# Kernel tuning notes

Hardware: AMD Instinct MI355X
Metric: run time of the kernel (lower is better)

The kernel has to match this reference:

```python
import jax, jax.numpy as jnp
import numpy as np

N_NODES = 100000
N_EDGES = 3200000
IN_DIM, HID_DIM, OUT_DIM = 128, 64, 2


def setup_inputs() -> dict:
    key = jax.random.key(0)
    k1, k2, k3, k4 = jax.random.split(key, 4)
    x = jax.random.normal(k1, (N_NODES, IN_DIM), dtype=jnp.float32)
    edge_index = jax.random.randint(k2, (2, N_EDGES), 0, N_NODES, dtype=jnp.int64)
    # GCNConv weights (glorot-style scale) and zero biases
    W1 = jax.random.normal(k3, (IN_DIM, HID_DIM), dtype=jnp.float32) / np.sqrt(IN_DIM)
    b1 = jnp.zeros((HID_DIM,), dtype=jnp.float32)
    W2 = jax.random.normal(k4, (HID_DIM, OUT_DIM), dtype=jnp.float32) / np.sqrt(HID_DIM)
    b2 = jnp.zeros((OUT_DIM,), dtype=jnp.float32)
    return {"x": x, "edge_index": edge_index, "W1": W1, "b1": b1, "W2": W2, "b2": b2}


def _gcn_norm(edge_index, num_nodes):
    # PyG GCNConv default: add self-loops, symmetric normalization deg^-1/2.
    loops = jnp.arange(num_nodes, dtype=edge_index.dtype)
    src = jnp.concatenate([edge_index[0], loops])  # [E+N]
    dst = jnp.concatenate([edge_index[1], loops])  # [E+N]
    deg = jax.ops.segment_sum(jnp.ones_like(dst, dtype=jnp.float32), dst,
                              num_segments=num_nodes)  # in-degree incl. self-loop
    dinv = jnp.where(deg > 0, jax.lax.rsqrt(deg), 0.0)
    norm = dinv[src] * dinv[dst]  # [E+N]
    return src, dst, norm


def _gcn_conv(h, W, b, src, dst, norm, num_nodes):
    h = h @ W                              # dense transform first (smaller dim)
    msg = h[src] * norm[:, None]           # gather + scale: [E+N, d]
    out = jax.ops.segment_sum(msg, dst, num_segments=num_nodes)  # scatter-add
    return out + b


def reference(x, edge_index, W1, b1, W2, b2):
    n = x.shape[0]
    src, dst, norm = _gcn_norm(edge_index, n)
    h = _gcn_conv(x, W1, b1, src, dst, norm, n)
    h = jax.nn.relu(h)
    return _gcn_conv(h, W2, b2, src, dst, norm, n)
```

## Files before the change

kernel.cpp:

```cpp
#include <hip/hip_runtime.h>
#include <hip/hip_bf16.h>


#define N_NODES 100000
#define IN_DIM 128
#define HID_DIM 64
#define OUT_DIM 2
#define NB 391
#define BCAP 12288
#define CROUNDS 12
#define CHUNK 8192
#define ZROW N_NODES

typedef short bf16x8 __attribute__((ext_vector_type(8)));
typedef float f32x4 __attribute__((ext_vector_type(4)));

__device__ __forceinline__ unsigned short f2bf(float x) {
    unsigned int u = __float_as_uint(x);
    unsigned int r = (u + 0x7FFFu + ((u >> 16) & 1u)) >> 16;
    return (unsigned short)r;
}
__device__ __forceinline__ float bflo(unsigned int u) { return __uint_as_float(u << 16); }
__device__ __forceinline__ float bfhi(unsigned int u) { return __uint_as_float(u & 0xFFFF0000u); }
__device__ __forceinline__ f32x4 vlo(uint4 r) {
    return (f32x4){bflo(r.x), bflo(r.y), bflo(r.z), bflo(r.w)};
}
__device__ __forceinline__ f32x4 vhi(uint4 r) {
    return (f32x4){bfhi(r.x), bfhi(r.y), bfhi(r.z), bfhi(r.w)};
}
__device__ __forceinline__ int wave_incl_scan(int v, int laneid) {
#pragma unroll
    for (int off = 1; off < 64; off <<= 1) {
        int u = __shfl_up(v, off);
        if (laneid >= off) v += u;
    }
    return v;
}

__global__ __launch_bounds__(512) void part_kernel(const int* __restrict__ ei,
                                                   int* __restrict__ gCursor,
                                                   int* __restrict__ part, int E) {
    __shared__ int hist[512], lrow[512], gbase[512], lcur[512];
    __shared__ int lpk[CHUNK];
    __shared__ short lbkt[CHUNK];
    __shared__ int wsum[8], wofs[8];
    const int t = threadIdx.x;
    const int lane = t & 63, wv = t >> 6;
    const int base = blockIdx.x * CHUNK;
    const int cntC = min(CHUNK, E - base);

    hist[t] = 0;
    __syncthreads();

    int s[16], d[16];
    bool val[16];
    if (base + CHUNK <= E) {
#pragma unroll
        for (int i = 0; i < 4; ++i) {
            int4 sv = ((const int4*)(ei + base))[t + i * 512];
            int4 dv = ((const int4*)(ei + E + base))[t + i * 512];
            s[i * 4 + 0] = sv.x; s[i * 4 + 1] = sv.y; s[i * 4 + 2] = sv.z; s[i * 4 + 3] = sv.w;
            d[i * 4 + 0] = dv.x; d[i * 4 + 1] = dv.y; d[i * 4 + 2] = dv.z; d[i * 4 + 3] = dv.w;
            val[i * 4 + 0] = val[i * 4 + 1] = val[i * 4 + 2] = val[i * 4 + 3] = true;
        }
    } else {
#pragma unroll
        for (int i = 0; i < 16; ++i) {
            int e = base + t + i * 512;
            val[i] = (e < E);
            if (val[i]) {
                s[i] = ei[e];
                d[i] = ei[E + e];
            }
        }
    }
#pragma unroll
    for (int i = 0; i < 16; ++i)
        if (val[i]) atomicAdd(&hist[d[i] >> 8], 1);
    __syncthreads();

    int v = hist[t];
    int inc = wave_incl_scan(v, lane);
    if (lane == 63) wsum[wv] = inc;
    __syncthreads();
    if (t < 64) {
        int w = (t < 8) ? wsum[t] : 0;
        int wi = wave_incl_scan(w, t);
        if (t < 8) wofs[t] = wi - w;
    }
    __syncthreads();
    int excl = inc - v + wofs[wv];
    if (t < NB && v > 0) {
        int old = atomicAdd(&gCursor[t], v);
        gbase[t] = t * BCAP + old;
    }
    lcur[t] = excl;
    lrow[t] = excl;
    __syncthreads();

#pragma unroll
    for (int i = 0; i < 16; ++i) {
        if (val[i]) {
            int b = d[i] >> 8;
            int pos = atomicAdd(&lcur[b], 1);
            lpk[pos] = s[i] | ((d[i] & 255) << 20);
            lbkt[pos] = (short)b;
        }
    }
    __syncthreads();

    for (int i = t; i < cntC; i += 512) {
        int b = lbkt[i];
        int g = gbase[b] + (i - lrow[b]);
        if (g < (b + 1) * BCAP)
            part[g] = lpk[i];
    }
}

__global__ __launch_bounds__(1024) void csr_kernel(const int* __restrict__ part,
                                                   const int* __restrict__ gCursor,
                                                   int* __restrict__ cnt,
                                                   float* __restrict__ dinv,
                                                   int* __restrict__ rowptr,
                                                   int* __restrict__ csr_src, int n) {
    __shared__ int wcnt[16][256];
    __shared__ int wsum[4], wofs[4];
    const int b = blockIdx.x, t = threadIdx.x;
    const int lane = t & 63, wv = t >> 6;
    const int start = b * BCAP;
    const int count = min(gCursor[b], BCAP);

    for (int i = t; i < 16 * 256; i += 1024) ((int*)wcnt)[i] = 0;
    __syncthreads();

    int pk[CROUNDS];
    bool val[CROUNDS];
#pragma unroll
    for (int k = 0; k < CROUNDS; ++k) {
        int i = t + k * 1024;
        val[k] = (i < count);
        pk[k] = val[k] ? part[start + i] : 0;
        if (val[k]) atomicAdd(&wcnt[wv][(pk[k] >> 20) & 255], 1);
    }
    __syncthreads();

    int v = 0, pv = 0;
    if (t < 256) {
        int sum = 0;
#pragma unroll
        for (int w = 0; w < 16; ++w) sum += wcnt[w][t];
        v = sum;
        pv = (v + 3) & ~3;
    }
    int inc = 0;
    if (t < 256) {
        inc = wave_incl_scan(pv, lane);
        if (lane == 63) wsum[wv] = inc;
    }
    __syncthreads();
    if (t < 64) {
        int w = (t < 4) ? wsum[t] : 0;
        int wi = wave_incl_scan(w, t);
        if (t < 4) wofs[t] = wi - w;
    }
    __syncthreads();
    if (t < 256) {
        int excl = inc - pv + wofs[wv];
        int node = (b << 8) + t;
        if (node < n) {
            cnt[node] = v;
            dinv[node] = rsqrtf((float)v + 1.0f);
            rowptr[node] = start + excl;
        }
        int run = excl;
#pragma unroll
        for (int w = 0; w < 16; ++w) {
            int c = wcnt[w][t];
            wcnt[w][t] = run;
            run += c;
        }
    }
    __syncthreads();

#pragma unroll
    for (int k = 0; k < CROUNDS; ++k) {
        if (val[k]) {
            int pos = atomicAdd(&wcnt[wv][(pk[k] >> 20) & 255], 1);
            csr_src[start + pos] = pk[k] & 0xFFFFF;
        }
    }
}

__global__ __launch_bounds__(256) void gemm1_kernel(const float* __restrict__ x,
                                                    const float* __restrict__ W1,
                                                    const float* __restrict__ dinv,
                                                    unsigned short* __restrict__ hsb, int n) {
    __shared__ unsigned short sX[64 * 136];
    __shared__ unsigned short sW[64 * 136];
    const int tid = threadIdx.x;
    const int rbase = blockIdx.x * 64;

    for (int i = tid; i < 2048; i += 256) {
        int k = i >> 4, cq = (i & 15) << 2;
        float4 v = ((const float4*)W1)[i];
        sW[(cq + 0) * 136 + k] = f2bf(v.x);
        sW[(cq + 1) * 136 + k] = f2bf(v.y);
        sW[(cq + 2) * 136 + k] = f2bf(v.z);
        sW[(cq + 3) * 136 + k] = f2bf(v.w);
    }
    for (int i = tid; i < 2048; i += 256) {
        int r = i >> 5, kq = (i & 31) << 2;
        int gr = rbase + r;
        float4 v = make_float4(0.f, 0.f, 0.f, 0.f);
        if (gr < n) v = ((const float4*)x)[gr * 32 + (i & 31)];
        ushort4 u;
        u.x = f2bf(v.x); u.y = f2bf(v.y); u.z = f2bf(v.z); u.w = f2bf(v.w);
        *(ushort4*)&sX[r * 136 + kq] = u;
    }
    __syncthreads();

    const int wave = tid >> 6, lane = tid & 63;
    const int quad = lane >> 4, l16 = lane & 15;
    const int rowoff = wave * 16;

    f32x4 acc[4];
#pragma unroll
    for (int t = 0; t < 4; ++t) acc[t] = (f32x4){0.f, 0.f, 0.f, 0.f};

#pragma unroll
    for (int k0 = 0; k0 < 128; k0 += 32) {
        bf16x8 a = *(const bf16x8*)&sX[(rowoff + l16) * 136 + k0 + quad * 8];
#pragma unroll
        for (int t = 0; t < 4; ++t) {
            bf16x8 b = *(const bf16x8*)&sW[(t * 16 + l16) * 136 + k0 + quad * 8];
            acc[t] = __builtin_amdgcn_mfma_f32_16x16x32_bf16(a, b, acc[t], 0, 0, 0);
        }
    }

#pragma unroll
    for (int r = 0; r < 4; ++r) {
        int grow = rbase + rowoff + quad * 4 + r;
        if (grow < n) {
            float di = dinv[grow];
#pragma unroll
            for (int t = 0; t < 4; ++t)
                hsb[grow * HID_DIM + t * 16 + l16] = f2bf(acc[t][r] * di);
        }
    }
}

__global__ __launch_bounds__(256) void agg1_kernel(const int* __restrict__ rowptr,
                                                   const int* __restrict__ cnt,
                                                   const int* __restrict__ csr_src,
                                                   const unsigned short* __restrict__ hsb,
                                                   const float* __restrict__ dinv,
                                                   const float* __restrict__ b1,
                                                   const float* __restrict__ W2,
                                                   float* __restrict__ hs2, int n) {
    const int node = blockIdx.x * 16 + (threadIdx.x >> 4);
    const int lane16 = threadIdx.x & 15;
    const int g = lane16 >> 3;
    const int l = lane16 & 7;
    const int start = rowptr[node];
    const int deg = cnt[node];
    const unsigned lofs = (unsigned)l * 8;

    f32x4 alo = (f32x4){0.f, 0.f, 0.f, 0.f};
    f32x4 ahi = (f32x4){0.f, 0.f, 0.f, 0.f};

    const int4* qp = (const int4*)csr_src + (start >> 2) + g;
    int4 cur = qp[0];
    int q = 0;
    for (;;) {
        const int e = q * 8 + 4 * g;
        const bool pf = (e + 8 < deg);
        int4 nxt = pf ? qp[2 * q + 2] : make_int4(ZROW, ZROW, ZROW, ZROW);
        int s0 = (e + 0 < deg) ? cur.x : ZROW;
        int s1 = (e + 1 < deg) ? cur.y : ZROW;
        int s2 = (e + 2 < deg) ? cur.z : ZROW;
        int s3 = (e + 3 < deg) ? cur.w : ZROW;
        uint4 r0 = *(const uint4*)&hsb[(unsigned)s0 * HID_DIM + lofs];
        uint4 r1 = *(const uint4*)&hsb[(unsigned)s1 * HID_DIM + lofs];
        uint4 r2 = *(const uint4*)&hsb[(unsigned)s2 * HID_DIM + lofs];
        uint4 r3 = *(const uint4*)&hsb[(unsigned)s3 * HID_DIM + lofs];
        alo += vlo(r0);  ahi += vhi(r0);
        alo += vlo(r1);  ahi += vhi(r1);
        alo += vlo(r2);  ahi += vhi(r2);
        alo += vlo(r3);  ahi += vhi(r3);
        cur = nxt;
        ++q;
        if (q * 8 >= deg) break;
    }

    float a[8];
    a[0] = alo[0]; a[1] = ahi[0]; a[2] = alo[1]; a[3] = ahi[1];
    a[4] = alo[2]; a[5] = ahi[2]; a[6] = alo[3]; a[7] = ahi[3];

#pragma unroll
    for (int i = 0; i < 8; ++i) a[i] += __shfl_xor(a[i], 8);

    {
        uint4 raw = *(const uint4*)&hsb[(unsigned)node * HID_DIM + lofs];
        a[0] += bflo(raw.x); a[1] += bfhi(raw.x);
        a[2] += bflo(raw.y); a[3] += bfhi(raw.y);
        a[4] += bflo(raw.z); a[5] += bfhi(raw.z);
        a[6] += bflo(raw.w); a[7] += bfhi(raw.w);
    }

    float di = dinv[node];
    float4 bb0 = *(const float4*)&b1[l * 8];
    float4 bb1 = *(const float4*)&b1[l * 8 + 4];
    float t0 = fmaxf(fmaf(di, a[0], bb0.x), 0.0f);
    float t1 = fmaxf(fmaf(di, a[1], bb0.y), 0.0f);
    float t2 = fmaxf(fmaf(di, a[2], bb0.z), 0.0f);
    float t3 = fmaxf(fmaf(di, a[3], bb0.w), 0.0f);
    float t4 = fmaxf(fmaf(di, a[4], bb1.x), 0.0f);
    float t5 = fmaxf(fmaf(di, a[5], bb1.y), 0.0f);
    float t6 = fmaxf(fmaf(di, a[6], bb1.z), 0.0f);
    float t7 = fmaxf(fmaf(di, a[7], bb1.w), 0.0f);

    float4 w0 = *(const float4*)&W2[l * 16];
    float4 w1 = *(const float4*)&W2[l * 16 + 4];
    float4 w2 = *(const float4*)&W2[l * 16 + 8];
    float4 w3 = *(const float4*)&W2[l * 16 + 12];
    float p0 = t0 * w0.x + t1 * w0.z + t2 * w1.x + t3 * w1.z
             + t4 * w2.x + t5 * w2.z + t6 * w3.x + t7 * w3.z;
    float p1 = t0 * w0.y + t1 * w0.w + t2 * w1.y + t3 * w1.w
             + t4 * w2.y + t5 * w2.w + t6 * w3.y + t7 * w3.w;
    p0 += __shfl_xor(p0, 1);  p1 += __shfl_xor(p1, 1);
    p0 += __shfl_xor(p0, 2);  p1 += __shfl_xor(p1, 2);
    p0 += __shfl_xor(p0, 4);  p1 += __shfl_xor(p1, 4);

    if (lane16 == 0) {
        *(float2*)&hs2[node * OUT_DIM] = make_float2(di * p0, di * p1);
    }
}

__global__ __launch_bounds__(256) void agg2_kernel(const int* __restrict__ rowptr,
                                                   const int* __restrict__ cnt,
                                                   const int* __restrict__ csr_src,
                                                   const float* __restrict__ hs2,
                                                   const float* __restrict__ dinv,
                                                   const float* __restrict__ b2,
                                                   float* __restrict__ out, int n) {
    int node = blockIdx.x * 8 + (threadIdx.x >> 5);
    if (node >= n) return;
    int lane = threadIdx.x & 31;
    int start = rowptr[node];
    int deg = cnt[node];

    float a0 = 0.0f, a1 = 0.0f;
    for (int j = lane; j < deg; j += 32) {
        int s = csr_src[start + j];
        float2 v = *(const float2*)&hs2[s * OUT_DIM];
        a0 += v.x;
        a1 += v.y;
    }
#pragma unroll
    for (int off = 16; off > 0; off >>= 1) {
        a0 += __shfl_xor(a0, off);
        a1 += __shfl_xor(a1, off);
    }
    if (lane == 0) {
        float di = dinv[node];
        float2 self = *(const float2*)&hs2[node * OUT_DIM];
        out[node * OUT_DIM + 0] = di * (a0 + self.x) + b2[0];
        out[node * OUT_DIM + 1] = di * (a1 + self.y) + b2[1];
    }
}

extern "C" void kernel_launch(void* const* d_in, const int* in_sizes, int n_in,
                              void* d_out, int out_size, void* d_ws, size_t ws_size,
                              hipStream_t stream) {
    const float* x  = (const float*)d_in[0];
    const int*   ei = (const int*)d_in[1];
    const float* W1 = (const float*)d_in[2];
    const float* b1 = (const float*)d_in[3];
    const float* W2 = (const float*)d_in[4];
    const float* b2 = (const float*)d_in[5];
    float* out = (float*)d_out;

    const int n = N_NODES;
    const int E = in_sizes[1] / 2;

    char* ws = (char*)d_ws;
    int*   gCursor = (int*)  (ws + 0);
    int*   cnt     = (int*)  (ws + (1u << 20));
    float* dinv    = (float*)(ws + (2u << 20));
    int*   rowptr  = (int*)  (ws + (3u << 20));
    float* hs2     = (float*)(ws + (4u << 20));
    int*   part    = (int*)  (ws + (5u << 20));
    unsigned short* hsb = (unsigned short*)(ws + (5u << 20));
    int*   csr_src = (int*)  (ws + (25u << 20));

    hipMemsetAsync(gCursor, 0, NB * sizeof(int), stream);

    part_kernel<<<(E + CHUNK - 1) / CHUNK, 512, 0, stream>>>(ei, gCursor, part, E);
    csr_kernel<<<NB, 1024, 0, stream>>>(part, gCursor, cnt, dinv, rowptr, csr_src, n);

    hipMemsetAsync(hsb + (size_t)N_NODES * HID_DIM, 0,
                   HID_DIM * sizeof(unsigned short), stream);

    gemm1_kernel<<<(n + 63) / 64, 256, 0, stream>>>(x, W1, dinv, hsb, n);
    agg1_kernel<<<n / 16, 256, 0, stream>>>(rowptr, cnt, csr_src, hsb, dinv, b1, W2, hs2, n);
    agg2_kernel<<<(n + 7) / 8, 256, 0, stream>>>(rowptr, cnt, csr_src, hs2, dinv, b2, out, n);
}
```

Baseline: 235.6 us.

## Pad CSR rows to 8 with zero-row sentinels and halve aggregation group sizes

CSR rows are now padded to multiples of 8, and the padding entries are filled with a sentinel pointing at a zeroed row. This lets agg1 drop the per-edge bounds checks and use 8 lanes per node, with each thread gathering 8 neighbors per iteration and no cross-group shuffle reduction. The zero row is now written inside gemm1 rather than by a separate memset. agg2 moves to 16 lanes per node. The changes aim to raise memory-level parallelism and cut control overhead, at the cost of more padded index traffic and larger per-thread serial chains on high-degree nodes.

```diff
diff --git a/kernel.cpp b/kernel.cpp
--- a/kernel.cpp
+++ b/kernel.cpp
@@ -150,7 +150,7 @@
 #pragma unroll
         for (int w = 0; w < 16; ++w) sum += wcnt[w][t];
         v = sum;
-        pv = (v + 3) & ~3;
+        pv = (v + 7) & ~7;
     }
     int inc = 0;
     if (t < 256) {
@@ -172,6 +172,7 @@
             dinv[node] = rsqrtf((float)v + 1.0f);
             rowptr[node] = start + excl;
         }
+        for (int j = v; j < pv; ++j) csr_src[start + excl + j] = ZROW;
         int run = excl;
 #pragma unroll
         for (int w = 0; w < 16; ++w) {
@@ -200,6 +201,9 @@
     const int tid = threadIdx.x;
     const int rbase = blockIdx.x * 64;
 
+    if (blockIdx.x == 0 && tid < 8)
+        ((float4*)&hsb[(unsigned)ZROW * HID_DIM])[tid] = make_float4(0.f, 0.f, 0.f, 0.f);
+
     for (int i = tid; i < 2048; i += 256) {
         int k = i >> 4, cq = (i & 15) << 2;
         float4 v = ((const float4*)W1)[i];
@@ -257,47 +261,45 @@
                                                    const float* __restrict__ b1,
                                                    const float* __restrict__ W2,
                                                    float* __restrict__ hs2, int n) {
-    const int node = blockIdx.x * 16 + (threadIdx.x >> 4);
-    const int lane16 = threadIdx.x & 15;
-    const int g = lane16 >> 3;
-    const int l = lane16 & 7;
+    const int node = blockIdx.x * 32 + (threadIdx.x >> 3);
+    const int l = threadIdx.x & 7;
+    const unsigned lofs = (unsigned)l * 8;
     const int start = rowptr[node];
     const int deg = cnt[node];
-    const unsigned lofs = (unsigned)l * 8;
+    const int iters = (deg + 7) >> 3;
 
     f32x4 alo = (f32x4){0.f, 0.f, 0.f, 0.f};
     f32x4 ahi = (f32x4){0.f, 0.f, 0.f, 0.f};
 
-    const int4* qp = (const int4*)csr_src + (start >> 2) + g;
-    int4 cur = qp[0];
-    int q = 0;
-    for (;;) {
-        const int e = q * 8 + 4 * g;
-        const bool pf = (e + 8 < deg);
-        int4 nxt = pf ? qp[2 * q + 2] : make_int4(ZROW, ZROW, ZROW, ZROW);
-        int s0 = (e + 0 < deg) ? cur.x : ZROW;
-        int s1 = (e + 1 < deg) ? cur.y : ZROW;
-        int s2 = (e + 2 < deg) ? cur.z : ZROW;
-        int s3 = (e + 3 < deg) ? cur.w : ZROW;
-        uint4 r0 = *(const uint4*)&hsb[(unsigned)s0 * HID_DIM + lofs];
-        uint4 r1 = *(const uint4*)&hsb[(unsigned)s1 * HID_DIM + lofs];
-        uint4 r2 = *(const uint4*)&hsb[(unsigned)s2 * HID_DIM + lofs];
-        uint4 r3 = *(const uint4*)&hsb[(unsigned)s3 * HID_DIM + lofs];
+    const int4* qp = (const int4*)(csr_src + start);
+    int4 ia = make_int4(ZROW, ZROW, ZROW, ZROW), ib = ia;
+    if (iters > 0) { ia = qp[0]; ib = qp[1]; }
+    for (int it = 0; it < iters; ++it) {
+        const bool more = (it + 1 < iters);
+        int4 na = more ? qp[2 * it + 2] : make_int4(ZROW, ZROW, ZROW, ZROW);
+        int4 nb = more ? qp[2 * it + 3] : make_int4(ZROW, ZROW, ZROW, ZROW);
+        uint4 r0 = *(const uint4*)&hsb[(unsigned)ia.x * HID_DIM + lofs];
+        uint4 r1 = *(const uint4*)&hsb[(unsigned)ia.y * HID_DIM + lofs];
+        uint4 r2 = *(const uint4*)&hsb[(unsigned)ia.z * HID_DIM + lofs];
+        uint4 r3 = *(const uint4*)&hsb[(unsigned)ia.w * HID_DIM + lofs];
+        uint4 r4 = *(const uint4*)&hsb[(unsigned)ib.x * HID_DIM + lofs];
+        uint4 r5 = *(const uint4*)&hsb[(unsigned)ib.y * HID_DIM + lofs];
+        uint4 r6 = *(const uint4*)&hsb[(unsigned)ib.z * HID_DIM + lofs];
+        uint4 r7 = *(const uint4*)&hsb[(unsigned)ib.w * HID_DIM + lofs];
         alo += vlo(r0);  ahi += vhi(r0);
         alo += vlo(r1);  ahi += vhi(r1);
         alo += vlo(r2);  ahi += vhi(r2);
         alo += vlo(r3);  ahi += vhi(r3);
-        cur = nxt;
-        ++q;
-        if (q * 8 >= deg) break;
+        alo += vlo(r4);  ahi += vhi(r4);
+        alo += vlo(r5);  ahi += vhi(r5);
+        alo += vlo(r6);  ahi += vhi(r6);
+        alo += vlo(r7);  ahi += vhi(r7);
+        ia = na; ib = nb;
     }
 
     float a[8];
     a[0] = alo[0]; a[1] = ahi[0]; a[2] = alo[1]; a[3] = ahi[1];
     a[4] = alo[2]; a[5] = ahi[2]; a[6] = alo[3]; a[7] = ahi[3];
-
-#pragma unroll
-    for (int i = 0; i < 8; ++i) a[i] += __shfl_xor(a[i], 8);
 
     {
         uint4 raw = *(const uint4*)&hsb[(unsigned)node * HID_DIM + lofs];
@@ -331,7 +333,7 @@
     p0 += __shfl_xor(p0, 2);  p1 += __shfl_xor(p1, 2);
     p0 += __shfl_xor(p0, 4);  p1 += __shfl_xor(p1, 4);
 
-    if (lane16 == 0) {
+    if (l == 0) {
         *(float2*)&hs2[node * OUT_DIM] = make_float2(di * p0, di * p1);
     }
 }
@@ -343,21 +345,20 @@
                                                    const float* __restrict__ dinv,
                                                    const float* __restrict__ b2,
                                                    float* __restrict__ out, int n) {
-    int node = blockIdx.x * 8 + (threadIdx.x >> 5);
-    if (node >= n) return;
-    int lane = threadIdx.x & 31;
+    int node = blockIdx.x * 16 + (threadIdx.x >> 4);
+    int lane = threadIdx.x & 15;
     int start = rowptr[node];
     int deg = cnt[node];
 
     float a0 = 0.0f, a1 = 0.0f;
-    for (int j = lane; j < deg; j += 32) {
+    for (int j = lane; j < deg; j += 16) {
         int s = csr_src[start + j];
         float2 v = *(const float2*)&hs2[s * OUT_DIM];
         a0 += v.x;
         a1 += v.y;
     }
 #pragma unroll
-    for (int off = 16; off > 0; off >>= 1) {
+    for (int off = 8; off > 0; off >>= 1) {
         a0 += __shfl_xor(a0, off);
         a1 += __shfl_xor(a1, off);
     }
@@ -398,10 +399,7 @@
     part_kernel<<<(E + CHUNK - 1) / CHUNK, 512, 0, stream>>>(ei, gCursor, part, E);
     csr_kernel<<<NB, 1024, 0, stream>>>(part, gCursor, cnt, dinv, rowptr, csr_src, n);
 
-    hipMemsetAsync(hsb + (size_t)N_NODES * HID_DIM, 0,
-                   HID_DIM * sizeof(unsigned short), stream);
-
     gemm1_kernel<<<(n + 63) / 64, 256, 0, stream>>>(x, W1, dinv, hsb, n);
-    agg1_kernel<<<n / 16, 256, 0, stream>>>(rowptr, cnt, csr_src, hsb, dinv, b1, W2, hs2, n);
-    agg2_kernel<<<(n + 7) / 8, 256, 0, stream>>>(rowptr, cnt, csr_src, hs2, dinv, b2, out, n);
-}
+    agg1_kernel<<<n / 32, 256, 0, stream>>>(rowptr, cnt, csr_src, hsb, dinv, b1, W2, hs2, n);
+    agg2_kernel<<<n / 16, 256, 0, stream>>>(rowptr, cnt, csr_src, hs2, dinv, b2, out, n);
+}
```

Measured after the change: 232.2 us. No clear change (-1.5%).
